# Optimization experiments

Hardware: AMD Instinct MI355X
Metric: run time of the kernel (lower is better)

## Reference

```python
import jax, jax.numpy as jnp
import numpy as np

# Production-scale dims inferred from the module (see shape_source)
B, S, M, H, D = 2, 2048, 1024, 16, 64  # batch, pos, d_model, n_heads, d_head
IGNORE = -1000.0  # value used by apply_causal_mask via self.IGNORE


def fp8_round(x):
    """Simulate per-tensor float8_e4m3fn quantize -> dequantize (FP8Manager is a
    straight dtype cast in the source: .to(float8_e4m3fn) then .to(float32))."""
    return x.astype(jnp.float8_e4m3fn).astype(jnp.float32)


def setup_inputs() -> dict:
    key = jax.random.key(0)
    ks = jax.random.split(key, 7)
    w_scale = jnp.float32(0.02)  # realistic transformer init scale
    return {
        "query_input": jax.random.normal(ks[0], (B, S, M), jnp.float32),
        "key_input":   jax.random.normal(ks[1], (B, S, M), jnp.float32),
        "value_input": jax.random.normal(ks[2], (B, S, M), jnp.float32),
        "W_Q": jax.random.normal(ks[3], (H, M, D), jnp.float32) * w_scale,
        "W_K": jax.random.normal(ks[4], (H, M, D), jnp.float32) * w_scale,
        "W_V": jax.random.normal(ks[5], (H, M, D), jnp.float32) * w_scale,
        "W_O": jax.random.normal(ks[6], (H, D, M), jnp.float32) * w_scale,
        "b_Q": jnp.zeros((H, D), jnp.float32),
        "b_K": jnp.zeros((H, D), jnp.float32),
        "b_V": jnp.zeros((H, D), jnp.float32),
        "b_O": jnp.zeros((M,), jnp.float32),
    }


def reference(query_input, key_input, value_input,
              W_Q, W_K, W_V, W_O, b_Q, b_K, b_V, b_O):
    # FP8-quantized QKV projections: activations and W_*_low are fp8_e4m3,
    # results are dequantized to float32 (fp8_matmul + FP8Manager.dequantize).
    q = jnp.einsum('bpm,hmd->bphd', fp8_round(query_input), fp8_round(W_Q)) + b_Q
    k = jnp.einsum('bpm,hmd->bphd', fp8_round(key_input),   fp8_round(W_K)) + b_K
    v = jnp.einsum('bpm,hmd->bphd', fp8_round(value_input), fp8_round(W_V)) + b_V

    attn_scale = jnp.float32(np.sqrt(D))  # cfg.use_attn_scale=True, layer scaling off
    scores = jnp.einsum('bqhd,bkhd->bhqk', q, k) / attn_scale  # [B,H,S,S]

    # causal mask (attn_type='global', attention_dir='causal'); masked -> IGNORE
    causal = jnp.tril(jnp.ones((S, S), dtype=bool))
    scores = jnp.where(causal[None, None], scores, jnp.float32(IGNORE))

    pattern = jax.nn.softmax(scores, axis=-1)
    z = jnp.einsum('bkhd,bhqk->bqhd', v, pattern)              # [B,S,H,D]
    out = jnp.einsum('bqhd,hdm->bqm', z, W_O) + b_O            # [B,S,M]
    return out
```

## Files before the change

### kernel.cpp

```cpp
#include <hip/hip_runtime.h>
#include <cstdint>
#include <cmath>

typedef __attribute__((ext_vector_type(4))) float f32x4;
typedef __attribute__((ext_vector_type(16))) float f32x16;
typedef __attribute__((ext_vector_type(8))) short bf16x8;
using u16 = unsigned short;
using u32 = uint32_t;


static __device__ __forceinline__ u16 f2bf(float f) {
  uint32_t u = __float_as_uint(f);
  u += 0x7fffu + ((u >> 16) & 1u);
  return (u16)(u >> 16);
}

static __device__ __forceinline__ float bf2f(u16 x) {
  return __uint_as_float((u32)x << 16);
}

static __device__ __forceinline__ float quant_e4m3(float x) {
  uint32_t u = __float_as_uint(x);
  uint32_t absu = u & 0x7fffffffu;
  if (absu >= 0x3c800000u) {
    uint32_t lsb = (absu >> 20) & 1u;
    uint32_t r = (absu + 0x7ffffu + lsb) & ~0xfffffu;
    return __uint_as_float((u & 0x80000000u) | r);
  }
  return rintf(x * 512.0f) * 0.001953125f;
}

static __device__ __forceinline__ void async16(const void* g, void* l) {
  __builtin_amdgcn_global_load_lds(
      (const __attribute__((address_space(1))) void*)g,
      (__attribute__((address_space(3))) void*)l, 16, 0, 0);
}

static __device__ __forceinline__ u32 cvtpk(float a, float b) {
  u32 r;
  asm("v_cvt_pk_bf16_f32 %0, %1, %2" : "=v"(r) : "v"(a), "v"(b));
  return r;
}

#define MFMA(a, b, c) __builtin_amdgcn_mfma_f32_16x16x32_bf16(a, b, c, 0, 0, 0)
#define MFMA32(a, b, c) __builtin_amdgcn_mfma_f32_32x32x16_bf16(a, b, c, 0, 0, 0)

#define QSCALE 0.18033688011112042f


__global__ __launch_bounds__(256)
void prep_kernel(const float* __restrict__ xq, const float* __restrict__ xk,
                 const float* __restrict__ xv,
                 u16* __restrict__ Xq, u16* __restrict__ Xk, u16* __restrict__ Xv,
                 const float* __restrict__ WQ, const float* __restrict__ WK,
                 const float* __restrict__ WV,
                 u16* __restrict__ WqT, u16* __restrict__ WkT, u16* __restrict__ WvT,
                 const float* __restrict__ WO, u16* __restrict__ WoT) {
  __shared__ u16 T[64][72];
  const int bid = blockIdx.x;
  const int t = threadIdx.x;

  if (bid < 6144) {
    const int which = bid >> 11, idx = bid & 2047;
    const float* x = which == 0 ? xq : (which == 1 ? xk : xv);
    u16* y = which == 0 ? Xq : (which == 1 ? Xk : Xv);
    int i = (idx * 256 + t) * 8;
    f32x4 a = *(const f32x4*)(x + i);
    f32x4 b = *(const f32x4*)(x + i + 4);
    union { bf16x8 v; u16 s[8]; } r;
#pragma unroll
    for (int j = 0; j < 4; ++j) r.s[j] = f2bf(quant_e4m3(a[j]));
#pragma unroll
    for (int j = 0; j < 4; ++j) r.s[4 + j] = f2bf(quant_e4m3(b[j]));
    *(bf16x8*)(y + i) = r.v;
    return;
  }

  if (bid < 6912) {
    const int sub = bid - 6144;
    const int zz = sub >> 8;
    const int rem = sub & 255;
    const int h = rem >> 4;
    const int k0 = (rem & 15) * 64;
    const float* w = zz == 0 ? WQ : (zz == 1 ? WK : WV);
    u16* wt = zz == 0 ? WqT : (zz == 1 ? WkT : WvT);
    int ml = t >> 2, d0 = (t & 3) * 16;
    const float* src = w + ((size_t)h * 1024 + (k0 + ml)) * 64 + d0;
    u16 q16[16];
#pragma unroll
    for (int j = 0; j < 16; j += 4) {
      f32x4 f = *(const f32x4*)(src + j);
#pragma unroll
      for (int c = 0; c < 4; ++c) q16[j + c] = f2bf(quant_e4m3(f[c]));
    }
#pragma unroll
    for (int j = 0; j < 16; ++j) T[ml][d0 + j] = q16[j];
    __syncthreads();
    int d = t >> 2, cb = t & 3;
    union { bf16x8 v; u16 s[8]; } o0, o1;
#pragma unroll
    for (int j = 0; j < 8; ++j) { o0.s[j] = T[cb * 16 + j][d]; o1.s[j] = T[cb * 16 + 8 + j][d]; }
    u16* dst = wt + (size_t)(h * 64 + d) * 1024 + k0 + cb * 16;
    *(bf16x8*)(dst) = o0.v;
    *(bf16x8*)(dst + 8) = o1.v;
    return;
  }

  {
    const int sub = bid - 6912;
    const int r0 = (sub >> 4) * 64;
    const int c0 = (sub & 15) * 64;
    int rl = t >> 2, cl0 = (t & 3) * 16;
    const float* src = WO + (size_t)(r0 + rl) * 1024 + c0 + cl0;
    u16 q16[16];
#pragma unroll
    for (int j = 0; j < 16; j += 4) {
      f32x4 f = *(const f32x4*)(src + j);
#pragma unroll
      for (int c = 0; c < 4; ++c) q16[j + c] = f2bf(f[c]);
    }
#pragma unroll
    for (int j = 0; j < 16; ++j) T[rl][cl0 + j] = q16[j];
    __syncthreads();
    int ml = t >> 2, cb = t & 3;
    union { bf16x8 v; u16 s[8]; } o0, o1;
#pragma unroll
    for (int j = 0; j < 8; ++j) { o0.s[j] = T[cb * 16 + j][ml]; o1.s[j] = T[cb * 16 + 8 + j][ml]; }
    u16* dst = WoT + (size_t)(c0 + ml) * 1024 + r0 + cb * 16;
    *(bf16x8*)(dst) = o0.v;
    *(bf16x8*)(dst + 8) = o1.v;
  }
}


__global__ __launch_bounds__(256)
void gemm_qkv_kernel(const u16* __restrict__ A0, const u16* __restrict__ A1, const u16* __restrict__ A2,
                     const u16* __restrict__ B0, const u16* __restrict__ B1, const u16* __restrict__ B2,
                     const float* __restrict__ bias0, const float* __restrict__ bias1,
                     const float* __restrict__ bias2,
                     u16* __restrict__ O0, u16* __restrict__ O1, u16* __restrict__ O2) {
  const int bz = blockIdx.z;
  const u16* Aptr = bz == 0 ? A0 : (bz == 1 ? A1 : A2);
  const u16* Bptr = bz == 0 ? B0 : (bz == 1 ? B1 : B2);
  const float* bias = bz == 0 ? bias0 : (bz == 1 ? bias1 : bias2);
  u16* O = bz == 0 ? O0 : (bz == 1 ? O1 : O2);

  __shared__ u16 As[5][128 * 32];
  __shared__ u16 Bs[5][128 * 32];
  const int m0 = blockIdx.x * 128;
  const int n0 = blockIdx.y * 128;
  const int tid = threadIdx.x;
  const int wave = tid >> 6, lane = tid & 63;
  const int wr = wave >> 1, wc = wave & 1;
  const int srow = lane >> 2;
  const int sgrp = (lane & 3) ^ ((lane >> 3) & 3);
  const int l15 = lane & 15;
  const int rg = (lane >> 4) ^ ((lane >> 1) & 3);

#define GSTAGE(KT, BUF)                                                       \
  {                                                                           \
    _Pragma("unroll") for (int j_ = 0; j_ < 2; ++j_) {                        \
      int c_ = wave * 2 + j_;                                                 \
      int row_ = c_ * 16 + srow;                                              \
      async16(Aptr + (size_t)(m0 + row_) * 1024 + (KT) + sgrp * 8,            \
              &As[BUF][c_ * 512]);                                            \
      async16(Bptr + (size_t)(n0 + row_) * 1024 + (KT) + sgrp * 8,            \
              &Bs[BUF][c_ * 512]);                                            \
    }                                                                         \
  }

  f32x4 acc[4][4] = {};

  GSTAGE(0, 0);
  GSTAGE(32, 1);
  GSTAGE(64, 2);
  GSTAGE(96, 3);
  asm volatile("s_waitcnt vmcnt(12)" ::: "memory");
  __builtin_amdgcn_s_barrier();

  int cur = 0;
  for (int it = 0; it < 32; ++it) {
    if (it + 4 < 32) GSTAGE((it + 4) * 32, (cur + 4) % 5);
    bf16x8 af[4], bfv[4];
#pragma unroll
    for (int i = 0; i < 4; ++i) {
      af[i] = *(const bf16x8*)(&As[cur][(wr * 64 + i * 16 + l15) * 32 + rg * 8]);
      bfv[i] = *(const bf16x8*)(&Bs[cur][(wc * 64 + i * 16 + l15) * 32 + rg * 8]);
    }
    __builtin_amdgcn_s_setprio(1);
#pragma unroll
    for (int i = 0; i < 4; ++i)
#pragma unroll
      for (int j = 0; j < 4; ++j)
        acc[i][j] = MFMA(af[i], bfv[j], acc[i][j]);
    __builtin_amdgcn_s_setprio(0);
    if (it + 1 < 32) {
      if (it + 4 < 32) {
        asm volatile("s_waitcnt vmcnt(12) lgkmcnt(0)" ::: "memory");
      } else if (it + 3 < 32) {
        asm volatile("s_waitcnt vmcnt(8) lgkmcnt(0)" ::: "memory");
      } else if (it + 2 < 32) {
        asm volatile("s_waitcnt vmcnt(4) lgkmcnt(0)" ::: "memory");
      } else {
        asm volatile("s_waitcnt vmcnt(0) lgkmcnt(0)" ::: "memory");
      }
      __builtin_amdgcn_s_barrier();
    }
    cur = (cur + 1) % 5;
  }
#undef GSTAGE

  if (bz == 0) {
#pragma unroll
    for (int fm = 0; fm < 4; ++fm) {
#pragma unroll
      for (int fn = 0; fn < 4; ++fn) {
        int n = n0 + wc * 64 + fn * 16 + l15;
        int hh = n >> 6, d = n & 63;
        float bv = bias[n];
#pragma unroll
        for (int i = 0; i < 4; ++i) {
          int m = m0 + wr * 64 + fm * 16 + (lane >> 4) * 4 + i;
          int b = m >> 11, s = m & 2047;
          O[(((size_t)b * 16 + hh) * 2048 + s) * 64 + d] = f2bf((acc[fm][fn][i] + bv) * QSCALE);
        }
      }
    }
  } else if (bz == 1) {
#pragma unroll
    for (int fm = 0; fm < 4; ++fm) {
#pragma unroll
      for (int fn = 0; fn < 4; ++fn) {
        int n = n0 + wc * 64 + fn * 16 + l15;
        int hh = n >> 6, d = n & 63;
        float bv = bias[n];
        int kkq = d >> 4, dh = (d >> 3) & 1, e = d & 7;
#pragma unroll
        for (int i = 0; i < 4; ++i) {
          int m = m0 + wr * 64 + fm * 16 + (lane >> 4) * 4 + i;
          int b = m >> 11, s = m & 2047;
          int bhh = b * 16 + hh;
          int T = s >> 6, rh = (s >> 5) & 1, ln = (s & 31) | (dh << 5);
          O[(size_t)bhh * 131072 + T * 4096 + rh * 2048 + kkq * 512 + ln * 8 + e] =
              f2bf(acc[fm][fn][i] + bv);
        }
      }
    }
  } else {
#pragma unroll
    for (int fm = 0; fm < 4; ++fm) {
#pragma unroll
      for (int fn = 0; fn < 4; ++fn) {
        int n = n0 + wc * 64 + fn * 16 + l15;
        int hh = n >> 6, d = n & 63;
        float bv = bias[n];
        int m_base = m0 + wr * 64 + fm * 16 + (lane >> 4) * 4;
        int b = m_base >> 11, s = m_base & 2047;
        int bhh = b * 16 + hh;
        int T = s >> 6, kkq = (s >> 4) & 3, sh = (s >> 3) & 1, e0 = s & 7;
        int ln = (d & 31) | (sh << 5), rh = d >> 5;
        union { u16 s4[4]; uint2 u2; } pk;
#pragma unroll
        for (int i = 0; i < 4; ++i) pk.s4[i] = f2bf(acc[fm][fn][i] + bv);
        *(uint2*)(&O[(size_t)bhh * 131072 + T * 4096 + rh * 2048 + kkq * 512 + ln * 8 + e0]) = pk.u2;
      }
    }
  }
}


__global__ __launch_bounds__(128, 4)
void attn_kernel(const u16* __restrict__ q, const u16* __restrict__ kfrag,
                 const u16* __restrict__ vfrag,
                 u16* __restrict__ PO, float* __restrict__ PM, float* __restrict__ PL) {
  const int bh = blockIdx.x, pr = blockIdx.y, zs = blockIdx.z;
  const int w = threadIdx.x >> 6, lane = threadIdx.x & 63;
  const int qi = w ? 63 - pr : pr;
  const int l31 = lane & 31, h = lane >> 5;
  const size_t base = (size_t)bh * 131072;
  const int wq0 = qi * 32;
  const int q_glob = wq0 + l31;
  const int NT = (wq0 + 95) >> 6;

  bf16x8 qf[4];
  {
    const u16* qp = q + base + (size_t)q_glob * 64 + 8 * h;
#pragma unroll
    for (int kk = 0; kk < 4; ++kk) qf[kk] = *(const bf16x8*)(qp + 16 * kk);
  }

  f32x16 oa0 = {}, oa1 = {};
  float mreg = -1e30f, lsum = 0.f;

  for (int T = zs; T < NT; T += 2) {
    const u16* kt = kfrag + base + (size_t)T * 4096;
    const u16* vt = vfrag + base + (size_t)T * 4096;
    bf16x8 kf0[4], kf1[4];
#pragma unroll
    for (int kk = 0; kk < 4; ++kk) {
      kf0[kk] = *(const bf16x8*)(kt + kk * 512 + lane * 8);
      kf1[kk] = *(const bf16x8*)(kt + 2048 + kk * 512 + lane * 8);
    }
    f32x16 sa0 = {}, sa1 = {};
    __builtin_amdgcn_s_setprio(1);
#pragma unroll
    for (int kk = 0; kk < 4; ++kk) {
      sa0 = MFMA32(kf0[kk], qf[kk], sa0);
      sa1 = MFMA32(kf1[kk], qf[kk], sa1);
    }
    __builtin_amdgcn_s_setprio(0);
    bf16x8 vf0[4], vf1[4];
#pragma unroll
    for (int kk = 0; kk < 4; ++kk) {
      vf0[kk] = *(const bf16x8*)(vt + kk * 512 + lane * 8);
      vf1[kk] = *(const bf16x8*)(vt + 2048 + kk * 512 + lane * 8);
    }

    const int kv0 = T * 64;
    if (kv0 + 63 > wq0) {
      int kvoff = kv0 + 4 * h - q_glob;
#pragma unroll
      for (int rr = 0; rr < 16; ++rr) {
        const int pat = (rr & 3) + 8 * (rr >> 2);
        if (pat + kvoff > 0) sa0[rr] = -1e30f;
        if (pat + 32 + kvoff > 0) sa1[rr] = -1e30f;
      }
    }

    float mx[8];
#pragma unroll
    for (int i = 0; i < 8; ++i)
      mx[i] = fmaxf(fmaxf(sa0[i], sa0[i + 8]), fmaxf(sa1[i], sa1[i + 8]));
    float pmax = fmaxf(fmaxf(fmaxf(mx[0], mx[1]), fmaxf(mx[2], mx[3])),
                       fmaxf(fmaxf(mx[4], mx[5]), fmaxf(mx[6], mx[7])));
    pmax = fmaxf(pmax, __shfl_xor(pmax, 32));

    if (!__all(pmax <= mreg + 8.f)) {
      float mnew = fmaxf(mreg, pmax);
      float alpha = __builtin_amdgcn_exp2f(mreg - mnew);
      mreg = mnew;
      lsum *= alpha;
#pragma unroll
      for (int i = 0; i < 16; ++i) { oa0[i] *= alpha; oa1[i] *= alpha; }
    }

    float rs[4] = {0.f, 0.f, 0.f, 0.f};
    u32 P32[2][4][2];
#pragma unroll
    for (int tt = 0; tt < 4; ++tt)
#pragma unroll
      for (int cc = 0; cc < 2; ++cc) {
        float p0 = __builtin_amdgcn_exp2f(sa0[4 * tt + 2 * cc] - mreg);
        float p1 = __builtin_amdgcn_exp2f(sa0[4 * tt + 2 * cc + 1] - mreg);
        float p2 = __builtin_amdgcn_exp2f(sa1[4 * tt + 2 * cc] - mreg);
        float p3 = __builtin_amdgcn_exp2f(sa1[4 * tt + 2 * cc + 1] - mreg);
        rs[tt] += (p0 + p1) + (p2 + p3);
        P32[0][tt][cc] = cvtpk(p0, p1);
        P32[1][tt][cc] = cvtpk(p2, p3);
      }
    float rsum = (rs[0] + rs[1]) + (rs[2] + rs[3]);
    rsum += __shfl_xor(rsum, 32);
    lsum += rsum;

    __builtin_amdgcn_s_setprio(1);
#pragma unroll
    for (int kk = 0; kk < 4; ++kk) {
      const int fp = kk >> 1;
      const int ta = 2 * (kk & 1);
      union { u32 u[4]; bf16x8 v; } pb;
#pragma unroll
      for (int cc = 0; cc < 2; ++cc) {
        u32 a = P32[fp][ta][cc], b = P32[fp][ta + 1][cc];
        asm("v_permlane32_swap_b32 %0, %1" : "+v"(a), "+v"(b));
        pb.u[cc] = a;
        pb.u[2 + cc] = b;
      }
      oa0 = MFMA32(vf0[kk], pb.v, oa0);
      oa1 = MFMA32(vf1[kk], pb.v, oa1);
    }
    __builtin_amdgcn_s_setprio(0);
  }

  const float inv = lsum > 0.f ? 1.f / lsum : 0.f;
  const size_t prow = (size_t)(zs * 32 + bh) * 2048 + q_glob;
  u16* pop = PO + prow * 64;
#pragma unroll
  for (int fd = 0; fd < 2; ++fd)
#pragma unroll
    for (int tt = 0; tt < 4; ++tt) {
      union { u16 s[4]; uint2 u2; } pk;
#pragma unroll
      for (int i = 0; i < 4; ++i) {
        float ov = (fd ? oa1[4 * tt + i] : oa0[4 * tt + i]) * inv;
        pk.s[i] = f2bf(ov);
      }
      *(uint2*)(pop + fd * 32 + tt * 8 + 4 * h) = pk.u2;
    }
  if (h == 0) {
    PM[prow] = mreg;
    PL[prow] = lsum;
  }
}


__global__ __launch_bounds__(256)
void combine_kernel(const u16* __restrict__ PO, const float* __restrict__ PM,
                    const float* __restrict__ PL, u16* __restrict__ z) {
  const int g = blockIdx.x * 256 + threadIdx.x;
  const int row = g >> 2, dp = (g & 3) * 16;
  const int bh = row >> 11, qq = row & 2047;
  const int b = bh >> 4, head = bh & 15;
  float m0 = PM[row], m1 = PM[65536 + row];
  float l0 = PL[row], l1 = PL[65536 + row];
  float m = fmaxf(m0, m1);
  float a0 = l0 * __builtin_amdgcn_exp2f(m0 - m);
  float a1 = l1 * __builtin_amdgcn_exp2f(m1 - m);
  float inv = 1.f / (a0 + a1);
  a0 *= inv; a1 *= inv;
  const u16* p0 = PO + (size_t)row * 64 + dp;
  const u16* p1 = PO + 4194304ull + (size_t)row * 64 + dp;
  union { bf16x8 v; u16 s[8]; } i0a, i0b, i1a, i1b, oA, oB;
  i0a.v = *(const bf16x8*)(p0);
  i0b.v = *(const bf16x8*)(p0 + 8);
  i1a.v = *(const bf16x8*)(p1);
  i1b.v = *(const bf16x8*)(p1 + 8);
#pragma unroll
  for (int j = 0; j < 8; ++j) {
    oA.s[j] = f2bf(bf2f(i0a.s[j]) * a0 + bf2f(i1a.s[j]) * a1);
    oB.s[j] = f2bf(bf2f(i0b.s[j]) * a0 + bf2f(i1b.s[j]) * a1);
  }
  u16* zp = z + (((size_t)b * 2048 + qq) * 16 + head) * 64 + dp;
  *(bf16x8*)(zp) = oA.v;
  *(bf16x8*)(zp + 8) = oB.v;
}


__global__ __launch_bounds__(256)
void gemm_out_kernel(const u16* __restrict__ Aptr, const u16* __restrict__ Bptr,
                     const float* __restrict__ bias, float* __restrict__ Out) {
  __shared__ u16 As[5][128 * 32];
  __shared__ u16 Bs[5][128 * 32];
  const int m0 = blockIdx.x * 128;
  const int n0 = blockIdx.y * 128;
  const int tid = threadIdx.x;
  const int wave = tid >> 6, lane = tid & 63;
  const int wr = wave >> 1, wc = wave & 1;
  const int srow = lane >> 2;
  const int sgrp = (lane & 3) ^ ((lane >> 3) & 3);
  const int l15 = lane & 15;
  const int rg = (lane >> 4) ^ ((lane >> 1) & 3);

#define GSTAGE(KT, BUF)                                                       \
  {                                                                           \
    _Pragma("unroll") for (int j_ = 0; j_ < 2; ++j_) {                        \
      int c_ = wave * 2 + j_;                                                 \
      int row_ = c_ * 16 + srow;                                              \
      async16(Aptr + (size_t)(m0 + row_) * 1024 + (KT) + sgrp * 8,            \
              &As[BUF][c_ * 512]);                                            \
      async16(Bptr + (size_t)(n0 + row_) * 1024 + (KT) + sgrp * 8,            \
              &Bs[BUF][c_ * 512]);                                            \
    }                                                                         \
  }

  f32x4 acc[4][4] = {};

  GSTAGE(0, 0);
  GSTAGE(32, 1);
  GSTAGE(64, 2);
  GSTAGE(96, 3);
  asm volatile("s_waitcnt vmcnt(12)" ::: "memory");
  __builtin_amdgcn_s_barrier();

  int cur = 0;
  for (int it = 0; it < 32; ++it) {
    if (it + 4 < 32) GSTAGE((it + 4) * 32, (cur + 4) % 5);
    bf16x8 af[4], bfv[4];
#pragma unroll
    for (int i = 0; i < 4; ++i) {
      af[i] = *(const bf16x8*)(&As[cur][(wr * 64 + i * 16 + l15) * 32 + rg * 8]);
      bfv[i] = *(const bf16x8*)(&Bs[cur][(wc * 64 + i * 16 + l15) * 32 + rg * 8]);
    }
    __builtin_amdgcn_s_setprio(1);
#pragma unroll
    for (int i = 0; i < 4; ++i)
#pragma unroll
      for (int j = 0; j < 4; ++j)
        acc[i][j] = MFMA(af[i], bfv[j], acc[i][j]);
    __builtin_amdgcn_s_setprio(0);
    if (it + 1 < 32) {
      if (it + 4 < 32) {
        asm volatile("s_waitcnt vmcnt(12) lgkmcnt(0)" ::: "memory");
      } else if (it + 3 < 32) {
        asm volatile("s_waitcnt vmcnt(8) lgkmcnt(0)" ::: "memory");
      } else if (it + 2 < 32) {
        asm volatile("s_waitcnt vmcnt(4) lgkmcnt(0)" ::: "memory");
      } else {
        asm volatile("s_waitcnt vmcnt(0) lgkmcnt(0)" ::: "memory");
      }
      __builtin_amdgcn_s_barrier();
    }
    cur = (cur + 1) % 5;
  }
#undef GSTAGE

#pragma unroll
  for (int fm = 0; fm < 4; ++fm) {
#pragma unroll
    for (int fn = 0; fn < 4; ++fn) {
      int n = n0 + wc * 64 + fn * 16 + l15;
      float bv = bias[n];
#pragma unroll
      for (int i = 0; i < 4; ++i) {
        int m = m0 + wr * 64 + fm * 16 + (lane >> 4) * 4 + i;
        Out[(size_t)m * 1024 + n] = acc[fm][fn][i] + bv;
      }
    }
  }
}


extern "C" void kernel_launch(void* const* d_in, const int* in_sizes, int n_in,
                              void* d_out, int out_size, void* d_ws, size_t ws_size,
                              hipStream_t stream) {
  const float* xq = (const float*)d_in[0];
  const float* xk = (const float*)d_in[1];
  const float* xv = (const float*)d_in[2];
  const float* WQ = (const float*)d_in[3];
  const float* WK = (const float*)d_in[4];
  const float* WV = (const float*)d_in[5];
  const float* WO = (const float*)d_in[6];
  const float* bQ = (const float*)d_in[7];
  const float* bK = (const float*)d_in[8];
  const float* bV = (const float*)d_in[9];
  const float* bO = (const float*)d_in[10];
  float* out = (float*)d_out;

  char* ws = (char*)d_ws;
  const size_t MB = 1024 * 1024;
  u16* Xq = (u16*)(ws);
  u16* Xk = (u16*)(ws + 8 * MB);
  u16* Xv = (u16*)(ws + 16 * MB);
  u16* WqT = (u16*)(ws + 24 * MB);
  u16* WkT = (u16*)(ws + 26 * MB);
  u16* WvT = (u16*)(ws + 28 * MB);
  u16* WoT = (u16*)(ws + 30 * MB);
  u16* Q = (u16*)(ws + 32 * MB);
  u16* Kf = (u16*)(ws + 40 * MB);
  u16* Vf = (u16*)(ws + 48 * MB);
  u16* Z = (u16*)(ws + 56 * MB);
  u16* PO = (u16*)(ws);
  float* PM = (float*)(ws + 16 * MB);
  float* PL = (float*)(ws + 17 * MB);

  prep_kernel<<<dim3(7168), 256, 0, stream>>>(xq, xk, xv, Xq, Xk, Xv,
                                              WQ, WK, WV, WqT, WkT, WvT, WO, WoT);
  gemm_qkv_kernel<<<dim3(32, 8, 3), 256, 0, stream>>>(Xq, Xk, Xv, WqT, WkT, WvT,
                                                      bQ, bK, bV, Q, Kf, Vf);
  attn_kernel<<<dim3(32, 32, 2), 128, 0, stream>>>(Q, Kf, Vf, PO, PM, PL);
  combine_kernel<<<dim3(1024), 256, 0, stream>>>(PO, PM, PL, Z);
  gemm_out_kernel<<<dim3(32, 8), 256, 0, stream>>>(Z, WoT, bO, out);
}
```

Before: 140.7 us.

## Pre-swizzle QKV GEMM operands into fragment layout and split attention KV four ways

The prep kernel now writes the quantized activations and transposed weights straight into MFMA fragment order. This lets the QKV GEMM skip LDS staging and barriers and load fragments from global memory into double-buffered registers. Attention now splits the KV range four ways instead of two, with four waves per block each handling two query segments. The combine kernel merges four partials, one of which is stored temporarily in the output buffer. The aim is to cut LDS traffic and sync overhead in the GEMM and to give attention more parallelism. The cost is uncached global fragment loads with no LDS reuse across waves, plus more partial-result traffic.

```diff
diff --git a/kernel.cpp b/kernel.cpp
--- a/kernel.cpp
+++ b/kernel.cpp
@@ -46,6 +46,7 @@
 #define MFMA32(a, b, c) __builtin_amdgcn_mfma_f32_32x32x16_bf16(a, b, c, 0, 0, 0)
 
 #define QSCALE 0.18033688011112042f
+
 
 
 __global__ __launch_bounds__(256)
@@ -65,6 +66,7 @@
     const float* x = which == 0 ? xq : (which == 1 ? xk : xv);
     u16* y = which == 0 ? Xq : (which == 1 ? Xk : Xv);
     int i = (idx * 256 + t) * 8;
+    int row = i >> 10, k = i & 1023;
     f32x4 a = *(const f32x4*)(x + i);
     f32x4 b = *(const f32x4*)(x + i + 4);
     union { bf16x8 v; u16 s[8]; } r;
@@ -72,7 +74,9 @@
     for (int j = 0; j < 4; ++j) r.s[j] = f2bf(quant_e4m3(a[j]));
 #pragma unroll
     for (int j = 0; j < 4; ++j) r.s[4 + j] = f2bf(quant_e4m3(b[j]));
-    *(bf16x8*)(y + i) = r.v;
+    u16* dst = y + ((size_t)(row >> 4) * 32 + (k >> 5)) * 512 +
+               (size_t)(((row & 15) | (((k >> 3) & 3) << 4))) * 8;
+    *(bf16x8*)(dst) = r.v;
     return;
   }
 
@@ -100,9 +104,13 @@
     union { bf16x8 v; u16 s[8]; } o0, o1;
 #pragma unroll
     for (int j = 0; j < 8; ++j) { o0.s[j] = T[cb * 16 + j][d]; o1.s[j] = T[cb * 16 + 8 + j][d]; }
-    u16* dst = wt + (size_t)(h * 64 + d) * 1024 + k0 + cb * 16;
-    *(bf16x8*)(dst) = o0.v;
-    *(bf16x8*)(dst + 8) = o1.v;
+    const int n = h * 64 + d;
+    const int kt = (k0 >> 5) + (cb >> 1);
+    const int kg0 = (2 * cb) & 3, kg1 = (2 * cb + 1) & 3;
+    u16* dst0 = wt + ((size_t)(n >> 4) * 32 + kt) * 512 + (size_t)(((n & 15) | (kg0 << 4))) * 8;
+    u16* dst1 = wt + ((size_t)(n >> 4) * 32 + kt) * 512 + (size_t)(((n & 15) | (kg1 << 4))) * 8;
+    *(bf16x8*)(dst0) = o0.v;
+    *(bf16x8*)(dst1) = o1.v;
     return;
   }
 
@@ -140,75 +148,49 @@
                      const float* __restrict__ bias2,
                      u16* __restrict__ O0, u16* __restrict__ O1, u16* __restrict__ O2) {
   const int bz = blockIdx.z;
-  const u16* Aptr = bz == 0 ? A0 : (bz == 1 ? A1 : A2);
-  const u16* Bptr = bz == 0 ? B0 : (bz == 1 ? B1 : B2);
+  const u16* Af = bz == 0 ? A0 : (bz == 1 ? A1 : A2);
+  const u16* Bf = bz == 0 ? B0 : (bz == 1 ? B1 : B2);
   const float* bias = bz == 0 ? bias0 : (bz == 1 ? bias1 : bias2);
   u16* O = bz == 0 ? O0 : (bz == 1 ? O1 : O2);
 
-  __shared__ u16 As[5][128 * 32];
-  __shared__ u16 Bs[5][128 * 32];
-  const int m0 = blockIdx.x * 128;
-  const int n0 = blockIdx.y * 128;
   const int tid = threadIdx.x;
   const int wave = tid >> 6, lane = tid & 63;
   const int wr = wave >> 1, wc = wave & 1;
-  const int srow = lane >> 2;
-  const int sgrp = (lane & 3) ^ ((lane >> 3) & 3);
+  const int m0 = blockIdx.x * 128, n0 = blockIdx.y * 128;
   const int l15 = lane & 15;
-  const int rg = (lane >> 4) ^ ((lane >> 1) & 3);
-
-#define GSTAGE(KT, BUF)                                                       \
-  {                                                                           \
-    _Pragma("unroll") for (int j_ = 0; j_ < 2; ++j_) {                        \
-      int c_ = wave * 2 + j_;                                                 \
-      int row_ = c_ * 16 + srow;                                              \
-      async16(Aptr + (size_t)(m0 + row_) * 1024 + (KT) + sgrp * 8,            \
-              &As[BUF][c_ * 512]);                                            \
-      async16(Bptr + (size_t)(n0 + row_) * 1024 + (KT) + sgrp * 8,            \
-              &Bs[BUF][c_ * 512]);                                            \
-    }                                                                         \
-  }
+
+  const u16* Ab = Af + ((size_t)((m0 >> 4) + wr * 4) * 32) * 512 + lane * 8;
+  const u16* Bb = Bf + ((size_t)((n0 >> 4) + wc * 4) * 32) * 512 + lane * 8;
 
   f32x4 acc[4][4] = {};
-
-  GSTAGE(0, 0);
-  GSTAGE(32, 1);
-  GSTAGE(64, 2);
-  GSTAGE(96, 3);
-  asm volatile("s_waitcnt vmcnt(12)" ::: "memory");
-  __builtin_amdgcn_s_barrier();
-
-  int cur = 0;
-  for (int it = 0; it < 32; ++it) {
-    if (it + 4 < 32) GSTAGE((it + 4) * 32, (cur + 4) % 5);
-    bf16x8 af[4], bfv[4];
-#pragma unroll
-    for (int i = 0; i < 4; ++i) {
-      af[i] = *(const bf16x8*)(&As[cur][(wr * 64 + i * 16 + l15) * 32 + rg * 8]);
-      bfv[i] = *(const bf16x8*)(&Bs[cur][(wc * 64 + i * 16 + l15) * 32 + rg * 8]);
-    }
-    __builtin_amdgcn_s_setprio(1);
-#pragma unroll
-    for (int i = 0; i < 4; ++i)
-#pragma unroll
-      for (int j = 0; j < 4; ++j)
-        acc[i][j] = MFMA(af[i], bfv[j], acc[i][j]);
-    __builtin_amdgcn_s_setprio(0);
-    if (it + 1 < 32) {
-      if (it + 4 < 32) {
-        asm volatile("s_waitcnt vmcnt(12) lgkmcnt(0)" ::: "memory");
-      } else if (it + 3 < 32) {
-        asm volatile("s_waitcnt vmcnt(8) lgkmcnt(0)" ::: "memory");
-      } else if (it + 2 < 32) {
-        asm volatile("s_waitcnt vmcnt(4) lgkmcnt(0)" ::: "memory");
-      } else {
-        asm volatile("s_waitcnt vmcnt(0) lgkmcnt(0)" ::: "memory");
-      }
-      __builtin_amdgcn_s_barrier();
-    }
-    cur = (cur + 1) % 5;
-  }
-#undef GSTAGE
+  bf16x8 aA[4], bA[4], aB[4], bB[4];
+
+#define LOADF(AA, BB, KT)                                              \
+  {                                                                    \
+    _Pragma("unroll") for (int i_ = 0; i_ < 4; ++i_) {                 \
+      AA[i_] = *(const bf16x8*)(Ab + i_ * 16384 + (KT) * 512);         \
+      BB[i_] = *(const bf16x8*)(Bb + i_ * 16384 + (KT) * 512);         \
+    }                                                                  \
+  }
+#define DOMFMA(AA, BB)                                                 \
+  {                                                                    \
+    __builtin_amdgcn_s_setprio(1);                                     \
+    _Pragma("unroll") for (int i_ = 0; i_ < 4; ++i_)                   \
+      _Pragma("unroll") for (int j_ = 0; j_ < 4; ++j_)                 \
+        acc[i_][j_] = MFMA(AA[i_], BB[j_], acc[i_][j_]);               \
+    __builtin_amdgcn_s_setprio(0);                                     \
+  }
+
+  LOADF(aA, bA, 0);
+#pragma unroll 2
+  for (int kt = 0; kt < 32; kt += 2) {
+    LOADF(aB, bB, kt + 1);
+    DOMFMA(aA, bA);
+    if (kt + 2 < 32) LOADF(aA, bA, kt + 2);
+    DOMFMA(aB, bB);
+  }
+#undef LOADF
+#undef DOMFMA
 
   if (bz == 0) {
 #pragma unroll
@@ -269,166 +251,184 @@
 }
 
 
-__global__ __launch_bounds__(128, 4)
+__global__ __launch_bounds__(256)
 void attn_kernel(const u16* __restrict__ q, const u16* __restrict__ kfrag,
                  const u16* __restrict__ vfrag,
-                 u16* __restrict__ PO, float* __restrict__ PM, float* __restrict__ PL) {
-  const int bh = blockIdx.x, pr = blockIdx.y, zs = blockIdx.z;
+                 u16* __restrict__ PO, u16* __restrict__ PO3,
+                 float* __restrict__ PM, float* __restrict__ PL) {
+  const int bh = blockIdx.x, zs = blockIdx.z;
   const int w = threadIdx.x >> 6, lane = threadIdx.x & 63;
-  const int qi = w ? 63 - pr : pr;
+  const int pr = blockIdx.y * 4 + w;
   const int l31 = lane & 31, h = lane >> 5;
   const size_t base = (size_t)bh * 131072;
-  const int wq0 = qi * 32;
-  const int q_glob = wq0 + l31;
-  const int NT = (wq0 + 95) >> 6;
-
-  bf16x8 qf[4];
-  {
-    const u16* qp = q + base + (size_t)q_glob * 64 + 8 * h;
-#pragma unroll
-    for (int kk = 0; kk < 4; ++kk) qf[kk] = *(const bf16x8*)(qp + 16 * kk);
-  }
-
-  f32x16 oa0 = {}, oa1 = {};
-  float mreg = -1e30f, lsum = 0.f;
-
-  for (int T = zs; T < NT; T += 2) {
-    const u16* kt = kfrag + base + (size_t)T * 4096;
-    const u16* vt = vfrag + base + (size_t)T * 4096;
-    bf16x8 kf0[4], kf1[4];
-#pragma unroll
-    for (int kk = 0; kk < 4; ++kk) {
-      kf0[kk] = *(const bf16x8*)(kt + kk * 512 + lane * 8);
-      kf1[kk] = *(const bf16x8*)(kt + 2048 + kk * 512 + lane * 8);
-    }
-    f32x16 sa0 = {}, sa1 = {};
-    __builtin_amdgcn_s_setprio(1);
-#pragma unroll
-    for (int kk = 0; kk < 4; ++kk) {
-      sa0 = MFMA32(kf0[kk], qf[kk], sa0);
-      sa1 = MFMA32(kf1[kk], qf[kk], sa1);
-    }
-    __builtin_amdgcn_s_setprio(0);
-    bf16x8 vf0[4], vf1[4];
-#pragma unroll
-    for (int kk = 0; kk < 4; ++kk) {
-      vf0[kk] = *(const bf16x8*)(vt + kk * 512 + lane * 8);
-      vf1[kk] = *(const bf16x8*)(vt + 2048 + kk * 512 + lane * 8);
-    }
-
-    const int kv0 = T * 64;
-    if (kv0 + 63 > wq0) {
-      int kvoff = kv0 + 4 * h - q_glob;
-#pragma unroll
-      for (int rr = 0; rr < 16; ++rr) {
-        const int pat = (rr & 3) + 8 * (rr >> 2);
-        if (pat + kvoff > 0) sa0[rr] = -1e30f;
-        if (pat + 32 + kvoff > 0) sa1[rr] = -1e30f;
-      }
-    }
-
-    float mx[8];
-#pragma unroll
-    for (int i = 0; i < 8; ++i)
-      mx[i] = fmaxf(fmaxf(sa0[i], sa0[i + 8]), fmaxf(sa1[i], sa1[i + 8]));
-    float pmax = fmaxf(fmaxf(fmaxf(mx[0], mx[1]), fmaxf(mx[2], mx[3])),
-                       fmaxf(fmaxf(mx[4], mx[5]), fmaxf(mx[6], mx[7])));
-    pmax = fmaxf(pmax, __shfl_xor(pmax, 32));
-
-    if (!__all(pmax <= mreg + 8.f)) {
-      float mnew = fmaxf(mreg, pmax);
-      float alpha = __builtin_amdgcn_exp2f(mreg - mnew);
-      mreg = mnew;
-      lsum *= alpha;
-#pragma unroll
-      for (int i = 0; i < 16; ++i) { oa0[i] *= alpha; oa1[i] *= alpha; }
-    }
-
-    float rs[4] = {0.f, 0.f, 0.f, 0.f};
-    u32 P32[2][4][2];
-#pragma unroll
-    for (int tt = 0; tt < 4; ++tt)
-#pragma unroll
-      for (int cc = 0; cc < 2; ++cc) {
-        float p0 = __builtin_amdgcn_exp2f(sa0[4 * tt + 2 * cc] - mreg);
-        float p1 = __builtin_amdgcn_exp2f(sa0[4 * tt + 2 * cc + 1] - mreg);
-        float p2 = __builtin_amdgcn_exp2f(sa1[4 * tt + 2 * cc] - mreg);
-        float p3 = __builtin_amdgcn_exp2f(sa1[4 * tt + 2 * cc + 1] - mreg);
-        rs[tt] += (p0 + p1) + (p2 + p3);
-        P32[0][tt][cc] = cvtpk(p0, p1);
-        P32[1][tt][cc] = cvtpk(p2, p3);
-      }
-    float rsum = (rs[0] + rs[1]) + (rs[2] + rs[3]);
-    rsum += __shfl_xor(rsum, 32);
-    lsum += rsum;
-
-    __builtin_amdgcn_s_setprio(1);
-#pragma unroll
-    for (int kk = 0; kk < 4; ++kk) {
-      const int fp = kk >> 1;
-      const int ta = 2 * (kk & 1);
-      union { u32 u[4]; bf16x8 v; } pb;
-#pragma unroll
-      for (int cc = 0; cc < 2; ++cc) {
-        u32 a = P32[fp][ta][cc], b = P32[fp][ta + 1][cc];
-        asm("v_permlane32_swap_b32 %0, %1" : "+v"(a), "+v"(b));
-        pb.u[cc] = a;
-        pb.u[2 + cc] = b;
-      }
-      oa0 = MFMA32(vf0[kk], pb.v, oa0);
-      oa1 = MFMA32(vf1[kk], pb.v, oa1);
-    }
-    __builtin_amdgcn_s_setprio(0);
-  }
-
-  const float inv = lsum > 0.f ? 1.f / lsum : 0.f;
-  const size_t prow = (size_t)(zs * 32 + bh) * 2048 + q_glob;
-  u16* pop = PO + prow * 64;
-#pragma unroll
-  for (int fd = 0; fd < 2; ++fd)
-#pragma unroll
-    for (int tt = 0; tt < 4; ++tt) {
-      union { u16 s[4]; uint2 u2; } pk;
-#pragma unroll
-      for (int i = 0; i < 4; ++i) {
-        float ov = (fd ? oa1[4 * tt + i] : oa0[4 * tt + i]) * inv;
-        pk.s[i] = f2bf(ov);
-      }
-      *(uint2*)(pop + fd * 32 + tt * 8 + 4 * h) = pk.u2;
-    }
-  if (h == 0) {
-    PM[prow] = mreg;
-    PL[prow] = lsum;
+
+#pragma unroll 1
+  for (int seg = 0; seg < 2; ++seg) {
+    const int qi = seg ? 63 - pr : pr;
+    const int wq0 = qi * 32;
+    const int q_glob = wq0 + l31;
+    const int NT = (wq0 + 95) >> 6;
+
+    bf16x8 qf[4];
+    {
+      const u16* qp = q + (size_t)bh * 131072 + (size_t)q_glob * 64 + 8 * h;
+#pragma unroll
+      for (int kk = 0; kk < 4; ++kk) qf[kk] = *(const bf16x8*)(qp + 16 * kk);
+    }
+
+    f32x16 oa0 = {}, oa1 = {};
+    float mreg = -1e30f, lsum = 0.f;
+
+    for (int T = zs; T < NT; T += 4) {
+      const u16* kt = kfrag + base + (size_t)T * 4096;
+      const u16* vt = vfrag + base + (size_t)T * 4096;
+      bf16x8 kf0[4], kf1[4];
+#pragma unroll
+      for (int kk = 0; kk < 4; ++kk) {
+        kf0[kk] = *(const bf16x8*)(kt + kk * 512 + lane * 8);
+        kf1[kk] = *(const bf16x8*)(kt + 2048 + kk * 512 + lane * 8);
+      }
+      f32x16 sa0 = {}, sa1 = {};
+      __builtin_amdgcn_s_setprio(1);
+#pragma unroll
+      for (int kk = 0; kk < 4; ++kk) {
+        sa0 = MFMA32(kf0[kk], qf[kk], sa0);
+        sa1 = MFMA32(kf1[kk], qf[kk], sa1);
+      }
+      __builtin_amdgcn_s_setprio(0);
+      bf16x8 vf0[4], vf1[4];
+#pragma unroll
+      for (int kk = 0; kk < 4; ++kk) {
+        vf0[kk] = *(const bf16x8*)(vt + kk * 512 + lane * 8);
+        vf1[kk] = *(const bf16x8*)(vt + 2048 + kk * 512 + lane * 8);
+      }
+
+      const int kv0 = T * 64;
+      if (kv0 + 63 > wq0) {
+        int kvoff = kv0 + 4 * h - q_glob;
+#pragma unroll
+        for (int rr = 0; rr < 16; ++rr) {
+          const int pat = (rr & 3) + 8 * (rr >> 2);
+          if (pat + kvoff > 0) sa0[rr] = -1e30f;
+          if (pat + 32 + kvoff > 0) sa1[rr] = -1e30f;
+        }
+      }
+
+      float mx[8];
+#pragma unroll
+      for (int i = 0; i < 8; ++i)
+        mx[i] = fmaxf(fmaxf(sa0[i], sa0[i + 8]), fmaxf(sa1[i], sa1[i + 8]));
+      float pmax = fmaxf(fmaxf(fmaxf(mx[0], mx[1]), fmaxf(mx[2], mx[3])),
+                         fmaxf(fmaxf(mx[4], mx[5]), fmaxf(mx[6], mx[7])));
+      pmax = fmaxf(pmax, __shfl_xor(pmax, 32));
+
+      if (!__all(pmax <= mreg + 8.f)) {
+        float mnew = fmaxf(mreg, pmax);
+        float alpha = __builtin_amdgcn_exp2f(mreg - mnew);
+        mreg = mnew;
+        lsum *= alpha;
+#pragma unroll
+        for (int i = 0; i < 16; ++i) { oa0[i] *= alpha; oa1[i] *= alpha; }
+      }
+
+      float rs[4] = {0.f, 0.f, 0.f, 0.f};
+      u32 P32[2][4][2];
+#pragma unroll
+      for (int tt = 0; tt < 4; ++tt)
+#pragma unroll
+        for (int cc = 0; cc < 2; ++cc) {
+          float p0 = __builtin_amdgcn_exp2f(sa0[4 * tt + 2 * cc] - mreg);
+          float p1 = __builtin_amdgcn_exp2f(sa0[4 * tt + 2 * cc + 1] - mreg);
+          float p2 = __builtin_amdgcn_exp2f(sa1[4 * tt + 2 * cc] - mreg);
+          float p3 = __builtin_amdgcn_exp2f(sa1[4 * tt + 2 * cc + 1] - mreg);
+          rs[tt] += (p0 + p1) + (p2 + p3);
+          P32[0][tt][cc] = cvtpk(p0, p1);
+          P32[1][tt][cc] = cvtpk(p2, p3);
+        }
+      float rsum = (rs[0] + rs[1]) + (rs[2] + rs[3]);
+      rsum += __shfl_xor(rsum, 32);
+      lsum += rsum;
+
+      __builtin_amdgcn_s_setprio(1);
+#pragma unroll
+      for (int kk = 0; kk < 4; ++kk) {
+        const int fp = kk >> 1;
+        const int ta = 2 * (kk & 1);
+        union { u32 u[4]; bf16x8 v; } pb;
+#pragma unroll
+        for (int cc = 0; cc < 2; ++cc) {
+          u32 a = P32[fp][ta][cc], b = P32[fp][ta + 1][cc];
+          asm("v_permlane32_swap_b32 %0, %1" : "+v"(a), "+v"(b));
+          pb.u[cc] = a;
+          pb.u[2 + cc] = b;
+        }
+        oa0 = MFMA32(vf0[kk], pb.v, oa0);
+        oa1 = MFMA32(vf1[kk], pb.v, oa1);
+      }
+      __builtin_amdgcn_s_setprio(0);
+    }
+
+    const float inv = lsum > 0.f ? 1.f / lsum : 0.f;
+    const size_t prow = (size_t)(zs * 32 + bh) * 2048 + q_glob;
+    u16* pop = (zs == 3) ? (PO3 + ((size_t)bh * 2048 + q_glob) * 64) : (PO + prow * 64);
+#pragma unroll
+    for (int fd = 0; fd < 2; ++fd)
+#pragma unroll
+      for (int tt = 0; tt < 4; ++tt) {
+        union { u16 s[4]; uint2 u2; } pk;
+#pragma unroll
+        for (int i = 0; i < 4; ++i) {
+          float ov = (fd ? oa1[4 * tt + i] : oa0[4 * tt + i]) * inv;
+          pk.s[i] = f2bf(ov);
+        }
+        *(uint2*)(pop + fd * 32 + tt * 8 + 4 * h) = pk.u2;
+      }
+    if (h == 0) {
+      PM[prow] = mreg;
+      PL[prow] = lsum;
+    }
   }
 }
 
 
 __global__ __launch_bounds__(256)
-void combine_kernel(const u16* __restrict__ PO, const float* __restrict__ PM,
-                    const float* __restrict__ PL, u16* __restrict__ z) {
+void combine_kernel(const u16* __restrict__ PO, const u16* __restrict__ PO3,
+                    const float* __restrict__ PM, const float* __restrict__ PL,
+                    u16* __restrict__ z) {
   const int g = blockIdx.x * 256 + threadIdx.x;
   const int row = g >> 2, dp = (g & 3) * 16;
   const int bh = row >> 11, qq = row & 2047;
   const int b = bh >> 4, head = bh & 15;
-  float m0 = PM[row], m1 = PM[65536 + row];
-  float l0 = PL[row], l1 = PL[65536 + row];
-  float m = fmaxf(m0, m1);
-  float a0 = l0 * __builtin_amdgcn_exp2f(m0 - m);
-  float a1 = l1 * __builtin_amdgcn_exp2f(m1 - m);
-  float inv = 1.f / (a0 + a1);
-  a0 *= inv; a1 *= inv;
-  const u16* p0 = PO + (size_t)row * 64 + dp;
-  const u16* p1 = PO + 4194304ull + (size_t)row * 64 + dp;
-  union { bf16x8 v; u16 s[8]; } i0a, i0b, i1a, i1b, oA, oB;
-  i0a.v = *(const bf16x8*)(p0);
-  i0b.v = *(const bf16x8*)(p0 + 8);
-  i1a.v = *(const bf16x8*)(p1);
-  i1b.v = *(const bf16x8*)(p1 + 8);
-#pragma unroll
-  for (int j = 0; j < 8; ++j) {
-    oA.s[j] = f2bf(bf2f(i0a.s[j]) * a0 + bf2f(i1a.s[j]) * a1);
-    oB.s[j] = f2bf(bf2f(i0b.s[j]) * a0 + bf2f(i1b.s[j]) * a1);
-  }
+  float mm0 = PM[row], mm1 = PM[65536 + row], mm2 = PM[131072 + row], mm3 = PM[196608 + row];
+  float ll0 = PL[row], ll1 = PL[65536 + row], ll2 = PL[131072 + row], ll3 = PL[196608 + row];
+  float m = fmaxf(fmaxf(mm0, mm1), fmaxf(mm2, mm3));
+  float a0 = ll0 * __builtin_amdgcn_exp2f(mm0 - m);
+  float a1 = ll1 * __builtin_amdgcn_exp2f(mm1 - m);
+  float a2 = ll2 * __builtin_amdgcn_exp2f(mm2 - m);
+  float a3 = ll3 * __builtin_amdgcn_exp2f(mm3 - m);
+  float inv = 1.f / (a0 + a1 + a2 + a3);
+  a0 *= inv; a1 *= inv; a2 *= inv; a3 *= inv;
+
+  float accA[8] = {}, accB[8] = {};
+#define ACCUM(PTR, W)                                                     \
+  {                                                                       \
+    union { bf16x8 v; u16 s[8]; } xa, xb;                                 \
+    xa.v = *(const bf16x8*)(PTR);                                         \
+    xb.v = *(const bf16x8*)((PTR) + 8);                                   \
+    _Pragma("unroll") for (int j = 0; j < 8; ++j) {                       \
+      accA[j] += bf2f(xa.s[j]) * (W);                                     \
+      accB[j] += bf2f(xb.s[j]) * (W);                                     \
+    }                                                                     \
+  }
+  ACCUM(PO + (size_t)row * 64 + dp, a0)
+  ACCUM(PO + 4194304ull + (size_t)row * 64 + dp, a1)
+  ACCUM(PO + 8388608ull + (size_t)row * 64 + dp, a2)
+  ACCUM(PO3 + (size_t)row * 64 + dp, a3)
+#undef ACCUM
+
+  union { bf16x8 v; u16 s[8]; } oA, oB;
+#pragma unroll
+  for (int j = 0; j < 8; ++j) { oA.s[j] = f2bf(accA[j]); oB.s[j] = f2bf(accB[j]); }
   u16* zp = z + (((size_t)b * 2048 + qq) * 16 + head) * 64 + dp;
   *(bf16x8*)(zp) = oA.v;
   *(bf16x8*)(zp + 8) = oB.v;
@@ -549,14 +549,15 @@
   u16* Vf = (u16*)(ws + 48 * MB);
   u16* Z = (u16*)(ws + 56 * MB);
   u16* PO = (u16*)(ws);
-  float* PM = (float*)(ws + 16 * MB);
-  float* PL = (float*)(ws + 17 * MB);
+  u16* PO3 = (u16*)out;
+  float* PM = (float*)(ws + 24 * MB);
+  float* PL = (float*)(ws + 25 * MB);
 
   prep_kernel<<<dim3(7168), 256, 0, stream>>>(xq, xk, xv, Xq, Xk, Xv,
                                               WQ, WK, WV, WqT, WkT, WvT, WO, WoT);
   gemm_qkv_kernel<<<dim3(32, 8, 3), 256, 0, stream>>>(Xq, Xk, Xv, WqT, WkT, WvT,
                                                       bQ, bK, bV, Q, Kf, Vf);
-  attn_kernel<<<dim3(32, 32, 2), 128, 0, stream>>>(Q, Kf, Vf, PO, PM, PL);
-  combine_kernel<<<dim3(1024), 256, 0, stream>>>(PO, PM, PL, Z);
+  attn_kernel<<<dim3(32, 8, 4), 256, 0, stream>>>(Q, Kf, Vf, PO, PO3, PM, PL);
+  combine_kernel<<<dim3(1024), 256, 0, stream>>>(PO, PO3, PM, PL, Z);
   gemm_out_kernel<<<dim3(32, 8), 256, 0, stream>>>(Z, WoT, bO, out);
 }
```

Result: faster. 129.8 us (-7.7%).
